# Kernel optimization log

Measured on AMD Instinct MI355X. Metric: run time of the kernel, lower is better.

Reference implementation:

```python
import jax, jax.numpy as jnp
import numpy as np

N_NODES = 100000
N_EDGES = 3200000
D_IN = 256
D_OUT = 256


def setup_inputs() -> dict:
    key = jax.random.key(0)
    k1, k2, k3, k4, k5 = jax.random.split(key, 5)
    X = jax.random.normal(k1, (N_NODES, D_IN), dtype=jnp.float32)
    A_rows = jax.random.randint(k2, (N_EDGES,), 0, N_NODES, dtype=jnp.int64)
    A_cols = jax.random.randint(k3, (N_EDGES,), 0, N_NODES, dtype=jnp.int64)
    A_vals = jax.random.uniform(k4, (N_EDGES,), dtype=jnp.float32)
    # Xavier-uniform init of nn.Linear(in_dim, out_dim, bias=False): W is [out, in]
    limit = float(np.sqrt(6.0 / (D_IN + D_OUT)))
    W = jax.random.uniform(k5, (D_OUT, D_IN), minval=-limit, maxval=limit,
                           dtype=jnp.float32)
    return {"X": X, "A_rows": A_rows, "A_cols": A_cols, "A_vals": A_vals, "W": W}


def reference(X, A_rows, A_cols, A_vals, W):
    # AX = A_coo @ X : gather source features, scale by edge value, scatter-add by row
    msgs = X[A_cols] * A_vals[:, None]                  # [E, D_in]
    AX = jax.ops.segment_sum(msgs, A_rows, num_segments=N_NODES)  # [N, D_in]
    # Linear (bias=False) then ReLU; dropout p=0.0 is identity
    H = jax.nn.relu(AX @ W.T)                           # [N, D_out]
    return H
```

## Files before the change

### kernel.cpp

```cpp
#include <hip/hip_runtime.h>
#include <hip/hip_bf16.h>

#define N_NODES 100000
#define N_EDGES 3200000
#define D 256
#define SHIFT 9
#define NB 196
#define EPB 4096

typedef __attribute__((ext_vector_type(8))) short short8;
typedef __attribute__((ext_vector_type(4))) float f32x4;

__device__ inline short bfbits(float x) {
    __hip_bfloat16 h = __float2bfloat16(x);
    return __builtin_bit_cast(short, h);
}

__device__ inline short8 load_cvt8(const float* __restrict__ p) {
    float4 a = *(const float4*)p;
    float4 b = *(const float4*)(p + 4);
    short8 r;
    r[0] = bfbits(a.x); r[1] = bfbits(a.y); r[2] = bfbits(a.z); r[3] = bfbits(a.w);
    r[4] = bfbits(b.x); r[5] = bfbits(b.y); r[6] = bfbits(b.z); r[7] = bfbits(b.w);
    return r;
}

__device__ inline int block_excl_scan_256(int c, int* wsum, int& total) {
    const int lane = threadIdx.x & 63, wid = threadIdx.x >> 6;
    int v = c;
    #pragma unroll
    for (int off = 1; off < 64; off <<= 1) {
        int u = __shfl_up(v, off);
        if (lane >= off) v += u;
    }
    if (lane == 63) wsum[wid] = v;
    __syncthreads();
    int w0 = wsum[0], w1 = wsum[1], w2 = wsum[2], w3 = wsum[3];
    total = w0 + w1 + w2 + w3;
    int wex = (wid > 0 ? w0 : 0) + (wid > 1 ? w1 : 0) + (wid > 2 ? w2 : 0);
    return wex + v - c;
}

__global__ __launch_bounds__(256) void bucket_hist(
    const int* __restrict__ rows, int* __restrict__ gcnt, int nE)
{
    __shared__ int h[NB];
    for (int i = threadIdx.x; i < NB; i += 256) h[i] = 0;
    __syncthreads();
    for (int e = blockIdx.x * 256 + threadIdx.x; e < nE; e += gridDim.x * 256)
        atomicAdd(&h[rows[e] >> SHIFT], 1);
    __syncthreads();
    for (int i = threadIdx.x; i < NB; i += 256)
        if (h[i]) atomicAdd(&gcnt[i], h[i]);
}

__global__ __launch_bounds__(256) void bucket_scan(
    const int* __restrict__ gcnt, int* __restrict__ bbase,
    int* __restrict__ gcursor, int* __restrict__ row_ptr)
{
    __shared__ int wsum[4];
    int c = (threadIdx.x < NB) ? gcnt[threadIdx.x] : 0;
    int total;
    int ex = block_excl_scan_256(c, wsum, total);
    if (threadIdx.x < NB) { bbase[threadIdx.x] = ex; gcursor[threadIdx.x] = ex; }
    if (threadIdx.x == 0) { bbase[NB] = total; row_ptr[N_NODES] = total; }
}

__global__ __launch_bounds__(256) void bucket_split(
    const int* __restrict__ rows, const int* __restrict__ cols,
    const float* __restrict__ vals, int* __restrict__ gcursor,
    int* __restrict__ brow, int2* __restrict__ bcv, int nE)
{
    __shared__ int cnt[256];
    __shared__ int startp[256];
    __shared__ int posp[256];
    __shared__ int gb[256];
    __shared__ int wsum[4];
    __shared__ int srow[EPB];
    __shared__ int2 scv[EPB];
    const int t  = threadIdx.x;
    const int e0 = blockIdx.x * EPB;

    cnt[t] = 0;
    __syncthreads();

    int   myrow[16];
    int   mycol[16];
    float myval[16];
    #pragma unroll
    for (int k = 0; k < 16; ++k) {
        int e = e0 + k * 256 + t;
        if (e < nE) {
            myrow[k] = rows[e]; mycol[k] = cols[e]; myval[k] = vals[e];
            atomicAdd(&cnt[myrow[k] >> SHIFT], 1);
        } else {
            myrow[k] = -1; mycol[k] = 0; myval[k] = 0.f;
        }
    }
    __syncthreads();

    int c = cnt[t];
    int total;
    int ex = block_excl_scan_256(c, wsum, total);
    startp[t] = ex;
    posp[t]   = ex;
    if (t < NB && c) gb[t] = atomicAdd(&gcursor[t], c);
    __syncthreads();

    #pragma unroll
    for (int k = 0; k < 16; ++k) {
        if (myrow[k] >= 0) {
            int b = myrow[k] >> SHIFT;
            int p = atomicAdd(&posp[b], 1);
            srow[p] = myrow[k];
            scv[p]  = make_int2(mycol[k], __float_as_int(myval[k]));
        }
    }
    __syncthreads();

    const int lane = t & 63, wid = t >> 6;
    for (int b = wid; b < NB; b += 4) {
        int cb = cnt[b];
        if (!cb) continue;
        int st = startp[b], g = gb[b];
        for (int i = lane; i < cb; i += 64) {
            brow[g + i] = srow[st + i];
            bcv[g + i]  = scv[st + i];
        }
    }
}

__global__ __launch_bounds__(256) void bucket_to_csr(
    const int* __restrict__ bbase, const int* __restrict__ brow,
    const int2* __restrict__ bcv, int* __restrict__ row_ptr,
    int2* __restrict__ cedge)
{
    __shared__ int hist[512];
    __shared__ int cur[512];
    __shared__ int wsum[4];
    const int t  = threadIdx.x;
    const int b  = blockIdx.x;
    const int r0 = b << SHIFT;
    const int s  = bbase[b], e = bbase[b + 1];

    hist[t] = 0; hist[t + 256] = 0;
    __syncthreads();
    for (int j = s + t; j < e; j += 256)
        atomicAdd(&hist[brow[j] - r0], 1);
    __syncthreads();

    int c0 = hist[2 * t], c1 = hist[2 * t + 1];
    int total;
    int ex = block_excl_scan_256(c0 + c1, wsum, total);
    cur[2 * t]     = s + ex;
    cur[2 * t + 1] = s + ex + c0;
    int r = r0 + 2 * t;
    if (r     < N_NODES) row_ptr[r]     = s + ex;
    if (r + 1 < N_NODES) row_ptr[r + 1] = s + ex + c0;
    __syncthreads();

    for (int j = s + t; j < e; j += 256) {
        int rr = brow[j];
        int p = atomicAdd(&cur[rr - r0], 1);
        cedge[p] = bcv[j];
    }
}

__global__ __launch_bounds__(256) void gemm_bf16(
    const float* __restrict__ X,
    const float* __restrict__ W,
    unsigned short* __restrict__ Y,
    int M)
{
    const int wid  = threadIdx.x >> 6;
    const int lane = threadIdx.x & 63;
    const int m0   = blockIdx.x * 64;
    const int n0   = wid * 64;
    const int lr   = lane & 15;
    const int ko   = (lane >> 4) * 8;

    f32x4 acc[4][4] = {};

    #pragma unroll
    for (int k0 = 0; k0 < 256; k0 += 32) {
        short8 bfrag[4], afrag[4];
        #pragma unroll
        for (int j = 0; j < 4; ++j)
            bfrag[j] = load_cvt8(W + (size_t)(n0 + j * 16 + lr) * 256 + k0 + ko);
        #pragma unroll
        for (int i = 0; i < 4; ++i) {
            int r = m0 + i * 16 + lr;
            if (r > M - 1) r = M - 1;
            afrag[i] = load_cvt8(X + (size_t)r * 256 + k0 + ko);
        }
        #pragma unroll
        for (int i = 0; i < 4; ++i)
            #pragma unroll
            for (int j = 0; j < 4; ++j)
                acc[i][j] = __builtin_amdgcn_mfma_f32_16x16x32_bf16(
                    afrag[i], bfrag[j], acc[i][j], 0, 0, 0);
    }

    #pragma unroll
    for (int i = 0; i < 4; ++i) {
        int rbase = m0 + i * 16 + (lane >> 4) * 4;
        #pragma unroll
        for (int rr = 0; rr < 4; ++rr) {
            int r = rbase + rr;
            if (r < M) {
                #pragma unroll
                for (int j = 0; j < 4; ++j)
                    Y[(size_t)r * 256 + n0 + j * 16 + lr] =
                        (unsigned short)bfbits(acc[i][j][rr]);
            }
        }
    }
}

__global__ __launch_bounds__(256) void spmm_gather_relu(
    const unsigned short* __restrict__ Y,
    const int* __restrict__ row_ptr,
    const int2* __restrict__ cedge,
    float* __restrict__ H)
{
    int row  = blockIdx.x * 4 + (threadIdx.x >> 6);
    int lane = threadIdx.x & 63;
    if (row >= N_NODES) return;
    int s = row_ptr[row];
    int e = row_ptr[row + 1];

    float4 acc = make_float4(0.f, 0.f, 0.f, 0.f);
    for (int base = s; base < e; base += 64) {
        int idx = base + lane;
        int2 q = make_int2(0, 0);
        if (idx < e) q = cedge[idx];
        int cnt = min(64, e - base);
        for (int j = 0; j < cnt; ++j) {
            int   cj = __shfl(q.x, j);
            float vj = __int_as_float(__shfl(q.y, j));
            ushort4 y4 = *(const ushort4*)(Y + (size_t)cj * 256 + lane * 4);
            acc.x += __uint_as_float((unsigned)y4.x << 16) * vj;
            acc.y += __uint_as_float((unsigned)y4.y << 16) * vj;
            acc.z += __uint_as_float((unsigned)y4.z << 16) * vj;
            acc.w += __uint_as_float((unsigned)y4.w << 16) * vj;
        }
    }
    float4 r;
    r.x = acc.x > 0.f ? acc.x : 0.f;
    r.y = acc.y > 0.f ? acc.y : 0.f;
    r.z = acc.z > 0.f ? acc.z : 0.f;
    r.w = acc.w > 0.f ? acc.w : 0.f;
    ((float4*)(H + (size_t)row * 256))[lane] = r;
}


extern "C" void kernel_launch(void* const* d_in, const int* in_sizes, int n_in,
                              void* d_out, int out_size, void* d_ws, size_t ws_size,
                              hipStream_t stream) {
    const float* X    = (const float*)d_in[0];
    const int*   rows = (const int*)d_in[1];
    const int*   cols = (const int*)d_in[2];
    const float* vals = (const float*)d_in[3];
    const float* W    = (const float*)d_in[4];
    float*       H    = (float*)d_out;

    char* ws = (char*)d_ws;
    unsigned short* Y       = (unsigned short*)(ws);
    int*            row_ptr = (int*)(ws + 51200000);
    int2*           cedge   = (int2*)(ws + 51600896);
    int*            brow    = (int*)(ws + 77200896);
    int2*           bcv     = (int2*)(ws + 90000896);
    int*            gcnt    = (int*)(ws + 115600896);
    int*            bbase   = (int*)(ws + 115601920);
    int*            gcursor = (int*)(ws + 115602944);

    hipMemsetAsync(gcnt, 0, NB * sizeof(int), stream);

    bucket_hist<<<256, 256, 0, stream>>>(rows, gcnt, N_EDGES);
    bucket_scan<<<1, 256, 0, stream>>>(gcnt, bbase, gcursor, row_ptr);
    bucket_split<<<(N_EDGES + EPB - 1) / EPB, 256, 0, stream>>>(
        rows, cols, vals, gcursor, brow, bcv, N_EDGES);
    bucket_to_csr<<<NB, 256, 0, stream>>>(bbase, brow, bcv, row_ptr, cedge);

    gemm_bf16<<<(N_NODES + 63) / 64, 256, 0, stream>>>(X, W, Y, N_NODES);

    spmm_gather_relu<<<(N_NODES + 3) / 4, 256, 0, stream>>>(Y, row_ptr, cedge, H);
}
```

Measured before the change: 485.0 us.

## Pack local row into column bits and unroll gather loop with scalar indices

```diff
diff --git a/kernel.cpp b/kernel.cpp
--- a/kernel.cpp
+++ b/kernel.cpp
@@ -69,14 +69,13 @@
 __global__ __launch_bounds__(256) void bucket_split(
     const int* __restrict__ rows, const int* __restrict__ cols,
     const float* __restrict__ vals, int* __restrict__ gcursor,
-    int* __restrict__ brow, int2* __restrict__ bcv, int nE)
+    int2* __restrict__ bcv, int nE)
 {
     __shared__ int cnt[256];
     __shared__ int startp[256];
     __shared__ int posp[256];
     __shared__ int gb[256];
     __shared__ int wsum[4];
-    __shared__ int srow[EPB];
     __shared__ int2 scv[EPB];
     const int t  = threadIdx.x;
     const int e0 = blockIdx.x * EPB;
@@ -112,8 +111,8 @@
         if (myrow[k] >= 0) {
             int b = myrow[k] >> SHIFT;
             int p = atomicAdd(&posp[b], 1);
-            srow[p] = myrow[k];
-            scv[p]  = make_int2(mycol[k], __float_as_int(myval[k]));
+            scv[p] = make_int2(((myrow[k] & 511) << 17) | mycol[k],
+                               __float_as_int(myval[k]));
         }
     }
     __syncthreads();
@@ -123,17 +122,14 @@
         int cb = cnt[b];
         if (!cb) continue;
         int st = startp[b], g = gb[b];
-        for (int i = lane; i < cb; i += 64) {
-            brow[g + i] = srow[st + i];
-            bcv[g + i]  = scv[st + i];
-        }
+        for (int i = lane; i < cb; i += 64)
+            bcv[g + i] = scv[st + i];
     }
 }
 
 __global__ __launch_bounds__(256) void bucket_to_csr(
-    const int* __restrict__ bbase, const int* __restrict__ brow,
-    const int2* __restrict__ bcv, int* __restrict__ row_ptr,
-    int2* __restrict__ cedge)
+    const int* __restrict__ bbase, const int2* __restrict__ bcv,
+    int* __restrict__ row_ptr, int2* __restrict__ cedge)
 {
     __shared__ int hist[512];
     __shared__ int cur[512];
@@ -146,7 +142,7 @@
     hist[t] = 0; hist[t + 256] = 0;
     __syncthreads();
     for (int j = s + t; j < e; j += 256)
-        atomicAdd(&hist[brow[j] - r0], 1);
+        atomicAdd(&hist[(unsigned)bcv[j].x >> 17], 1);
     __syncthreads();
 
     int c0 = hist[2 * t], c1 = hist[2 * t + 1];
@@ -160,9 +156,10 @@
     __syncthreads();
 
     for (int j = s + t; j < e; j += 256) {
-        int rr = brow[j];
-        int p = atomicAdd(&cur[rr - r0], 1);
-        cedge[p] = bcv[j];
+        int2 q = bcv[j];
+        int rl = (unsigned)q.x >> 17;
+        int p = atomicAdd(&cur[rl], 1);
+        cedge[p] = make_int2(q.x & 0x1FFFF, q.y);
     }
 }
 
@@ -230,15 +227,48 @@
     int e = row_ptr[row + 1];
 
     float4 acc = make_float4(0.f, 0.f, 0.f, 0.f);
+    const int fo = lane * 4;
+
     for (int base = s; base < e; base += 64) {
         int idx = base + lane;
         int2 q = make_int2(0, 0);
         if (idx < e) q = cedge[idx];
         int cnt = min(64, e - base);
-        for (int j = 0; j < cnt; ++j) {
-            int   cj = __shfl(q.x, j);
-            float vj = __int_as_float(__shfl(q.y, j));
-            ushort4 y4 = *(const ushort4*)(Y + (size_t)cj * 256 + lane * 4);
+        int j = 0;
+        for (; j + 4 <= cnt; j += 4) {
+            int c0 = __builtin_amdgcn_readfirstlane(__shfl(q.x, j));
+            int c1 = __builtin_amdgcn_readfirstlane(__shfl(q.x, j + 1));
+            int c2 = __builtin_amdgcn_readfirstlane(__shfl(q.x, j + 2));
+            int c3 = __builtin_amdgcn_readfirstlane(__shfl(q.x, j + 3));
+            float v0 = __int_as_float(__builtin_amdgcn_readfirstlane(__shfl(q.y, j)));
+            float v1 = __int_as_float(__builtin_amdgcn_readfirstlane(__shfl(q.y, j + 1)));
+            float v2 = __int_as_float(__builtin_amdgcn_readfirstlane(__shfl(q.y, j + 2)));
+            float v3 = __int_as_float(__builtin_amdgcn_readfirstlane(__shfl(q.y, j + 3)));
+            ushort4 y0 = *(const ushort4*)(Y + (size_t)c0 * 256 + fo);
+            ushort4 y1 = *(const ushort4*)(Y + (size_t)c1 * 256 + fo);
+            ushort4 y2 = *(const ushort4*)(Y + (size_t)c2 * 256 + fo);
+            ushort4 y3 = *(const ushort4*)(Y + (size_t)c3 * 256 + fo);
+            acc.x += __uint_as_float((unsigned)y0.x << 16) * v0;
+            acc.y += __uint_as_float((unsigned)y0.y << 16) * v0;
+            acc.z += __uint_as_float((unsigned)y0.z << 16) * v0;
+            acc.w += __uint_as_float((unsigned)y0.w << 16) * v0;
+            acc.x += __uint_as_float((unsigned)y1.x << 16) * v1;
+            acc.y += __uint_as_float((unsigned)y1.y << 16) * v1;
+            acc.z += __uint_as_float((unsigned)y1.z << 16) * v1;
+            acc.w += __uint_as_float((unsigned)y1.w << 16) * v1;
+            acc.x += __uint_as_float((unsigned)y2.x << 16) * v2;
+            acc.y += __uint_as_float((unsigned)y2.y << 16) * v2;
+            acc.z += __uint_as_float((unsigned)y2.z << 16) * v2;
+            acc.w += __uint_as_float((unsigned)y2.w << 16) * v2;
+            acc.x += __uint_as_float((unsigned)y3.x << 16) * v3;
+            acc.y += __uint_as_float((unsigned)y3.y << 16) * v3;
+            acc.z += __uint_as_float((unsigned)y3.z << 16) * v3;
+            acc.w += __uint_as_float((unsigned)y3.w << 16) * v3;
+        }
+        for (; j < cnt; ++j) {
+            int   cj = __builtin_amdgcn_readfirstlane(__shfl(q.x, j));
+            float vj = __int_as_float(__builtin_amdgcn_readfirstlane(__shfl(q.y, j)));
+            ushort4 y4 = *(const ushort4*)(Y + (size_t)cj * 256 + fo);
             acc.x += __uint_as_float((unsigned)y4.x << 16) * vj;
             acc.y += __uint_as_float((unsigned)y4.y << 16) * vj;
             acc.z += __uint_as_float((unsigned)y4.z << 16) * vj;
@@ -268,19 +298,18 @@
     unsigned short* Y       = (unsigned short*)(ws);
     int*            row_ptr = (int*)(ws + 51200000);
     int2*           cedge   = (int2*)(ws + 51600896);
-    int*            brow    = (int*)(ws + 77200896);
-    int2*           bcv     = (int2*)(ws + 90000896);
-    int*            gcnt    = (int*)(ws + 115600896);
-    int*            bbase   = (int*)(ws + 115601920);
-    int*            gcursor = (int*)(ws + 115602944);
+    int2*           bcv     = (int2*)(ws + 77200896);
+    int*            gcnt    = (int*)(ws + 102800896);
+    int*            bbase   = (int*)(ws + 102801920);
+    int*            gcursor = (int*)(ws + 102802944);
 
     hipMemsetAsync(gcnt, 0, NB * sizeof(int), stream);
 
     bucket_hist<<<256, 256, 0, stream>>>(rows, gcnt, N_EDGES);
     bucket_scan<<<1, 256, 0, stream>>>(gcnt, bbase, gcursor, row_ptr);
     bucket_split<<<(N_EDGES + EPB - 1) / EPB, 256, 0, stream>>>(
-        rows, cols, vals, gcursor, brow, bcv, N_EDGES);
-    bucket_to_csr<<<NB, 256, 0, stream>>>(bbase, brow, bcv, row_ptr, cedge);
+        rows, cols, vals, gcursor, bcv, N_EDGES);
+    bucket_to_csr<<<NB, 256, 0, stream>>>(bbase, bcv, row_ptr, cedge);
 
     gemm_bf16<<<(N_NODES + 63) / 64, 256, 0, stream>>>(X, W, Y, N_NODES);
 
```

New measurement: 451.2 us. -7.0%, faster.
